# Optimization experiments

Measured on AMD Instinct MI355X. Metric: run time of the kernel, lower is better.

Reference implementation:

```python
import jax, jax.numpy as jnp
import numpy as np
import math

D_MODEL = 1024
NUM_HEADS = 16
D_K = D_MODEL // NUM_HEADS
B, S = 4, 2048


def setup_inputs() -> dict:
    key = jax.random.key(0)
    ks = jax.random.split(key, 12)
    q = jax.random.normal(ks[0], (B, S, D_MODEL), dtype=jnp.float32)
    k = jax.random.normal(ks[1], (B, S, D_MODEL), dtype=jnp.float32)
    v = jax.random.normal(ks[2], (B, S, D_MODEL), dtype=jnp.float32)
    # causal mask: True where attention is disallowed (masked_fill semantics)
    mask = jnp.triu(jnp.ones((S, S), dtype=bool), k=1)
    # xavier_uniform_ for projection weights, torch Linear default for biases
    limit = math.sqrt(6.0 / (D_MODEL + D_MODEL))
    def xavier(kk):
        return jax.random.uniform(kk, (D_MODEL, D_MODEL), jnp.float32, -limit, limit)
    blim = 1.0 / math.sqrt(D_MODEL)
    def bias(kk):
        return jax.random.uniform(kk, (D_MODEL,), jnp.float32, -blim, blim)
    return {
        "q": q, "k": k, "v": v, "mask": mask,
        "wq": xavier(ks[3]), "bq": bias(ks[4]),
        "wk": xavier(ks[5]), "bk": bias(ks[6]),
        "wv": xavier(ks[7]), "bv": bias(ks[8]),
        "wo": xavier(ks[9]), "bo": bias(ks[10]),
    }


def reference(q, k, v, mask, wq, bq, wk, bk, wv, bv, wo, bo):
    b = q.shape[0]
    # torch Linear: y = x @ W.T + b
    def proj(x, w, bb):
        return (jnp.einsum('bsd,ed->bse', x, w) + bb).reshape(b, -1, NUM_HEADS, D_K).transpose(0, 2, 1, 3)
    qh = proj(q, wq, bq)  # [B,H,S,d_k]
    kh = proj(k, wk, bk)
    vh = proj(v, wv, bv)
    scores = jnp.einsum('bhqd,bhkd->bhqk', qh, kh) / math.sqrt(D_K)
    scores = jnp.where(mask, jnp.float32(-1e9), scores)
    probs = jax.nn.softmax(scores, axis=-1)  # dropout p=0 -> identity
    out = jnp.einsum('bhqk,bhkd->bhqd', probs, vh)
    out = out.transpose(0, 2, 1, 3).reshape(b, -1, D_MODEL)
    return jnp.einsum('bsd,ed->bse', out, wo) + bo
```

## Files before the change

kernel.cpp:

```cpp
#include <hip/hip_runtime.h>
#include <hip/hip_bf16.h>
#include <math.h>

#define S_LEN 2048
#define DM    1024
#define NH    16
#define DKH   64
#define NEG_BIG (-1e30f)
#define QSCALE 0.18033688f

typedef __bf16 bf16_t;
typedef bf16_t bf16x8 __attribute__((ext_vector_type(8)));
typedef bf16_t bf16x4 __attribute__((ext_vector_type(4)));
typedef bf16_t bf16x2 __attribute__((ext_vector_type(2)));
typedef float  f32x4  __attribute__((ext_vector_type(4)));

__device__ __forceinline__ void gload16(const void* g, void* l) {
    __builtin_amdgcn_global_load_lds((const __attribute__((address_space(1))) void*)g,
                                     (__attribute__((address_space(3))) void*)l, 16, 0, 0);
}

__device__ __forceinline__ unsigned pack2(float a, float b) {
    bf16x2 v; v[0] = (bf16_t)a; v[1] = (bf16_t)b;
    return __builtin_bit_cast(unsigned, v);
}

__device__ __forceinline__ bf16x8 cvt8v(f32x4 a, f32x4 b) {
    bf16x8 v;
    v[0] = (bf16_t)a[0]; v[1] = (bf16_t)a[1]; v[2] = (bf16_t)a[2]; v[3] = (bf16_t)a[3];
    v[4] = (bf16_t)b[0]; v[5] = (bf16_t)b[1]; v[6] = (bf16_t)b[2]; v[7] = (bf16_t)b[3];
    return v;
}

__global__ __launch_bounds__(256) void cvt4_w(const float* __restrict__ w0, const float* __restrict__ w1,
                                              const float* __restrict__ w2, const float* __restrict__ w3,
                                              bf16_t* __restrict__ o0, bf16_t* __restrict__ o1,
                                              bf16_t* __restrict__ o2, bf16_t* __restrict__ o3) {
    const float* in; bf16_t* out;
    switch (blockIdx.y) {
        case 0: in = w0; out = o0; break;
        case 1: in = w1; out = o1; break;
        case 2: in = w2; out = o2; break;
        default: in = w3; out = o3; break;
    }
    int i = (blockIdx.x * 256 + threadIdx.x) * 4;
    float4 f = *(const float4*)(in + i);
    bf16x4 v;
    v[0] = (bf16_t)f.x; v[1] = (bf16_t)f.y; v[2] = (bf16_t)f.z; v[3] = (bf16_t)f.w;
    *(bf16x4*)(out + i) = v;
}

template<int EPI>
__global__ __launch_bounds__(256) void gemm_proj(const float* __restrict__ Af,
                                                 const bf16_t* __restrict__ B,
                                                 const float* __restrict__ bias,
                                                 bf16_t* __restrict__ Out,
                                                 float oscale) {
    __shared__ float  AsF[128 * 32];
    __shared__ bf16_t Bs[128 * 32];

    const int d    = blockIdx.x;
    const int orig = (d & 7) * 64 + (d >> 3);
    const int mBase = (orig >> 3) * 128;
    const int nBase = (orig & 7) * 128;

    const int tid  = threadIdx.x;
    const int w    = tid >> 6;
    const int lane = tid & 63;
    const int g    = lane >> 4;
    const int r    = lane & 15;
    const int wm   = w >> 1, wn = w & 1;

    const int srow = lane >> 2;
    const int scol = (lane & 3) * 8;
    const int frow = lane >> 3;
    const int fsl  = (lane & 7) ^ (frow & 7);

    f32x4 acc[4][4] = {};

    for (int kt = 0; kt < 1024; kt += 32) {
        #pragma unroll
        for (int c = 0; c < 4; ++c) {
            const int row = w * 32 + c * 8;
            gload16(Af + (size_t)(mBase + row + frow) * 1024 + kt + fsl * 4, &AsF[row * 32]);
        }
        #pragma unroll
        for (int c = 0; c < 2; ++c) {
            const int row = w * 32 + c * 16;
            gload16(B + (size_t)(nBase + row + srow) * 1024 + kt + scol, &Bs[row * 32]);
        }
        __syncthreads();

        bf16x8 af[4], bfr[4];
        #pragma unroll
        for (int i = 0; i < 4; i++) {
            const int R = wm * 64 + i * 16 + r;
            const float* rb = &AsF[R * 32];
            f32x4 f0 = *(const f32x4*)(rb + (((2 * g) ^ (r & 7)) << 2));
            f32x4 f1 = *(const f32x4*)(rb + (((2 * g + 1) ^ (r & 7)) << 2));
            af[i] = cvt8v(f0, f1);
        }
        #pragma unroll
        for (int i = 0; i < 4; i++)
            bfr[i] = *(const bf16x8*)&Bs[(wn * 64 + i * 16 + r) * 32 + g * 8];

        #pragma unroll
        for (int mi = 0; mi < 4; mi++)
            #pragma unroll
            for (int ni = 0; ni < 4; ni++)
                acc[mi][ni] = __builtin_amdgcn_mfma_f32_16x16x32_bf16(
                    af[mi], bfr[ni], acc[mi][ni], 0, 0, 0);
        __syncthreads();
    }

    #pragma unroll
    for (int ni = 0; ni < 4; ni++) {
        const int n = nBase + wn * 64 + ni * 16 + r;
        const float bn = bias[n];
        #pragma unroll
        for (int mi = 0; mi < 4; mi++) {
            #pragma unroll
            for (int qq = 0; qq < 4; qq++) {
                int m = mBase + wm * 64 + mi * 16 + g * 4 + qq;
                float val = (acc[mi][ni][qq] + bn) * oscale;
                int b = m >> 11, s = m & 2047;
                int hh = n >> 6, dd = n & 63;
                bf16_t bvv = (bf16_t)val;
                if constexpr (EPI == 0)
                    Out[(((size_t)(b * NH + hh)) * S_LEN + s) * DKH + dd] = bvv;
                else
                    Out[(((size_t)(b * NH + hh)) * DKH + dd) * S_LEN + s] = bvv;
            }
        }
    }
}

__global__ __launch_bounds__(256) void gemm_o(const bf16_t* __restrict__ A,
                                              const bf16_t* __restrict__ B,
                                              const float* __restrict__ bias,
                                              float* __restrict__ Out) {
    __shared__ bf16_t As[128 * 32];
    __shared__ bf16_t Bs[128 * 32];

    const int d    = blockIdx.x;
    const int orig = (d & 7) * 64 + (d >> 3);
    const int mBase = (orig >> 3) * 128;
    const int nBase = (orig & 7) * 128;

    const int tid  = threadIdx.x;
    const int w    = tid >> 6;
    const int lane = tid & 63;
    const int g    = lane >> 4;
    const int r    = lane & 15;
    const int wm   = w >> 1, wn = w & 1;

    const int srow = lane >> 2;
    const int scol = (lane & 3) * 8;

    f32x4 acc[4][4] = {};

    for (int kt = 0; kt < 1024; kt += 32) {
        #pragma unroll
        for (int c = 0; c < 2; ++c) {
            const int row = w * 32 + c * 16;
            gload16(A + (size_t)(mBase + row + srow) * 1024 + kt + scol, &As[row * 32]);
            gload16(B + (size_t)(nBase + row + srow) * 1024 + kt + scol, &Bs[row * 32]);
        }
        __syncthreads();

        bf16x8 af[4], bfr[4];
        #pragma unroll
        for (int i = 0; i < 4; i++)
            af[i] = *(const bf16x8*)&As[(wm * 64 + i * 16 + r) * 32 + g * 8];
        #pragma unroll
        for (int i = 0; i < 4; i++)
            bfr[i] = *(const bf16x8*)&Bs[(wn * 64 + i * 16 + r) * 32 + g * 8];

        #pragma unroll
        for (int mi = 0; mi < 4; mi++)
            #pragma unroll
            for (int ni = 0; ni < 4; ni++)
                acc[mi][ni] = __builtin_amdgcn_mfma_f32_16x16x32_bf16(
                    af[mi], bfr[ni], acc[mi][ni], 0, 0, 0);
        __syncthreads();
    }

    #pragma unroll
    for (int ni = 0; ni < 4; ni++) {
        const int n = nBase + wn * 64 + ni * 16 + r;
        const float bn = bias[n];
        #pragma unroll
        for (int mi = 0; mi < 4; mi++) {
            #pragma unroll
            for (int qq = 0; qq < 4; qq++) {
                int m = mBase + wm * 64 + mi * 16 + g * 4 + qq;
                Out[(size_t)m * 1024 + n] = acc[mi][ni][qq] + bn;
            }
        }
    }
}

__device__ __forceinline__ void tile_softmax(f32x4 s[4], bool diag, int kbase, int qg,
                                             int g, int srcA, int srcB, bool hi,
                                             bf16x8 pf[2]) {
    unsigned P32[8];
    #pragma unroll
    for (int ni = 0; ni < 4; ++ni) {
        float p[4];
        #pragma unroll
        for (int e = 0; e < 4; ++e) {
            float xx = s[ni][e];
            if (diag) {
                int kk = kbase + ni * 16 + g * 4 + e;
                if (kk > qg) xx = NEG_BIG;
            }
            p[e] = __builtin_amdgcn_exp2f(xx);
        }
        P32[2 * ni]     = pack2(p[0], p[1]);
        P32[2 * ni + 1] = pack2(p[2], p[3]);
    }
    unsigned A0 = __shfl(P32[0], srcA), A1 = __shfl(P32[1], srcA);
    unsigned A2 = __shfl(P32[2], srcA), A3 = __shfl(P32[3], srcA);
    unsigned A4 = __shfl(P32[4], srcA), A5 = __shfl(P32[5], srcA);
    unsigned A6 = __shfl(P32[6], srcA), A7 = __shfl(P32[7], srcA);
    unsigned B0 = __shfl(P32[0], srcB), B1 = __shfl(P32[1], srcB);
    unsigned B2 = __shfl(P32[2], srcB), B3 = __shfl(P32[3], srcB);
    unsigned B4 = __shfl(P32[4], srcB), B5 = __shfl(P32[5], srcB);
    unsigned B6 = __shfl(P32[6], srcB), B7 = __shfl(P32[7], srcB);
    union U { unsigned u[4]; bf16x8 v; } u0, u1;
    u0.u[0] = hi ? A2 : A0;  u0.u[1] = hi ? A3 : A1;
    u0.u[2] = hi ? B2 : B0;  u0.u[3] = hi ? B3 : B1;
    u1.u[0] = hi ? A6 : A4;  u1.u[1] = hi ? A7 : A5;
    u1.u[2] = hi ? B6 : B4;  u1.u[3] = hi ? B7 : B5;
    pf[0] = u0.v;
    pf[1] = u1.v;
}

__global__ __launch_bounds__(256) void attn8_kernel(const bf16_t* __restrict__ Qh,
                                                    const bf16_t* __restrict__ Kh,
                                                    const bf16_t* __restrict__ Vt,
                                                    bf16_t* __restrict__ Out) {
    __shared__ bf16_t KV[2][2][64][64];

    const int j   = blockIdx.x;
    const int c   = j >> 8;
    const int rem = j & 255;
    const int y   = rem >> 6;
    const int bh  = rem & 63;
    const int p   = (c == 0) ? y : (c == 1) ? 15 - y : (c == 2) ? 4 + y : 11 - y;

    const int b   = bh >> 4, h = bh & 15;
    const int tid = threadIdx.x;
    const int w    = tid >> 6;
    const int lane = tid & 63;
    const int g    = lane >> 4;
    const int r    = lane & 15;

    const int qtA = 2 * p, qtB = 2 * p + 1, last = qtB;

    const int srcA = 32 * (g & 1) + r;
    const int srcB = srcA + 16;
    const bool hi  = (g >= 2);

    const bf16_t* Qg = Qh + (size_t)bh * S_LEN * DKH;
    const bf16_t* Kg = Kh + (size_t)bh * S_LEN * DKH;
    const bf16_t* Vg = Vt + (size_t)bh * DKH * S_LEN;

    const int qA = qtA * 64 + w * 16 + r;
    const int qB = qtB * 64 + w * 16 + r;

    bf16x8 qfA[2], qfB[2];
    #pragma unroll
    for (int hh = 0; hh < 2; ++hh) {
        qfA[hh] = *(const bf16x8*)(Qg + (size_t)qA * DKH + hh * 32 + g * 8);
        qfB[hh] = *(const bf16x8*)(Qg + (size_t)qB * DKH + hh * 32 + g * 8);
    }

    bf16x8 ones;
    #pragma unroll
    for (int jj = 0; jj < 8; ++jj) ones[jj] = (bf16_t)1.0f;

    auto stage = [&](int buf, int kt) {
        #pragma unroll
        for (int cc = 0; cc < 2; ++cc) {
            const int row = w * 16 + cc * 8 + (lane >> 3);
            const int sl  = (lane & 7) ^ (row & 7);
            gload16(Kg + ((size_t)(kt * 64 + row)) * DKH + sl * 8,
                    (char*)&KV[buf][0][0][0] + w * 2048 + cc * 1024);
            gload16(Vg + (size_t)row * S_LEN + kt * 64 + sl * 8,
                    (char*)&KV[buf][1][0][0] + w * 2048 + cc * 1024);
        }
    };

    f32x4 oA[4] = {}, oB[4] = {};
    f32x4 lA4 = {}, lB4 = {};

    stage(0, 0);
    asm volatile("s_waitcnt vmcnt(0)" ::: "memory");
    __builtin_amdgcn_s_barrier();

    for (int kt = 0; kt <= last; ++kt) {
        const int buf = kt & 1;
        if (kt < last) stage(buf ^ 1, kt + 1);

        bf16x8 kf[4][2];
        #pragma unroll
        for (int ni = 0; ni < 4; ++ni) {
            const int row = ni * 16 + r;
            const char* base = (const char*)&KV[buf][0][0][0] + (row << 7);
            kf[ni][0] = *(const bf16x8*)(base + (((0 + g) ^ (row & 7)) << 4));
            kf[ni][1] = *(const bf16x8*)(base + (((4 + g) ^ (row & 7)) << 4));
        }

        const bool actA = (kt <= qtA);
        bf16x8 pfA[2], pfB[2];

        if (actA) {
            f32x4 s[4] = {};
            __builtin_amdgcn_s_setprio(1);
            #pragma unroll
            for (int ni = 0; ni < 4; ++ni) {
                s[ni] = __builtin_amdgcn_mfma_f32_16x16x32_bf16(kf[ni][0], qfA[0], s[ni], 0, 0, 0);
                s[ni] = __builtin_amdgcn_mfma_f32_16x16x32_bf16(kf[ni][1], qfA[1], s[ni], 0, 0, 0);
            }
            __builtin_amdgcn_s_setprio(0);
            tile_softmax(s, kt == qtA, kt * 64, qA, g, srcA, srcB, hi, pfA);
        }
        {
            f32x4 s[4] = {};
            __builtin_amdgcn_s_setprio(1);
            #pragma unroll
            for (int ni = 0; ni < 4; ++ni) {
                s[ni] = __builtin_amdgcn_mfma_f32_16x16x32_bf16(kf[ni][0], qfB[0], s[ni], 0, 0, 0);
                s[ni] = __builtin_amdgcn_mfma_f32_16x16x32_bf16(kf[ni][1], qfB[1], s[ni], 0, 0, 0);
            }
            __builtin_amdgcn_s_setprio(0);
            tile_softmax(s, kt == qtB, kt * 64, qB, g, srcA, srcB, hi, pfB);
        }

        __builtin_amdgcn_s_setprio(1);
        #pragma unroll
        for (int ndi = 0; ndi < 4; ++ndi) {
            const int row = ndi * 16 + r;
            const char* base = (const char*)&KV[buf][1][0][0] + (row << 7);
            bf16x8 v0 = *(const bf16x8*)(base + (((0 + g) ^ (row & 7)) << 4));
            bf16x8 v1 = *(const bf16x8*)(base + (((4 + g) ^ (row & 7)) << 4));
            if (actA) {
                oA[ndi] = __builtin_amdgcn_mfma_f32_16x16x32_bf16(v0, pfA[0], oA[ndi], 0, 0, 0);
                oA[ndi] = __builtin_amdgcn_mfma_f32_16x16x32_bf16(v1, pfA[1], oA[ndi], 0, 0, 0);
            }
            oB[ndi] = __builtin_amdgcn_mfma_f32_16x16x32_bf16(v0, pfB[0], oB[ndi], 0, 0, 0);
            oB[ndi] = __builtin_amdgcn_mfma_f32_16x16x32_bf16(v1, pfB[1], oB[ndi], 0, 0, 0);
        }
        if (actA) {
            lA4 = __builtin_amdgcn_mfma_f32_16x16x32_bf16(ones, pfA[0], lA4, 0, 0, 0);
            lA4 = __builtin_amdgcn_mfma_f32_16x16x32_bf16(ones, pfA[1], lA4, 0, 0, 0);
        }
        lB4 = __builtin_amdgcn_mfma_f32_16x16x32_bf16(ones, pfB[0], lB4, 0, 0, 0);
        lB4 = __builtin_amdgcn_mfma_f32_16x16x32_bf16(ones, pfB[1], lB4, 0, 0, 0);
        __builtin_amdgcn_s_setprio(0);

        asm volatile("s_waitcnt vmcnt(0)" ::: "memory");
        __builtin_amdgcn_s_barrier();
    }

    const float invA = 1.0f / lA4[0], invB = 1.0f / lB4[0];
    bf16_t* OutA = Out + ((size_t)(b * S_LEN + qA)) * DM + h * DKH;
    bf16_t* OutB = Out + ((size_t)(b * S_LEN + qB)) * DM + h * DKH;
    #pragma unroll
    for (int ndi = 0; ndi < 4; ++ndi) {
        bf16x4 pa, pb;
        #pragma unroll
        for (int e = 0; e < 4; ++e) {
            pa[e] = (bf16_t)(oA[ndi][e] * invA);
            pb[e] = (bf16_t)(oB[ndi][e] * invB);
        }
        *(bf16x4*)(OutA + ndi * 16 + g * 4) = pa;
        *(bf16x4*)(OutB + ndi * 16 + g * 4) = pb;
    }
}

extern "C" void kernel_launch(void* const* d_in, const int* in_sizes, int n_in,
                              void* d_out, int out_size, void* d_ws, size_t ws_size,
                              hipStream_t stream) {
    const float* q  = (const float*)d_in[0];
    const float* k  = (const float*)d_in[1];
    const float* v  = (const float*)d_in[2];
    const float* wq = (const float*)d_in[4];
    const float* bq = (const float*)d_in[5];
    const float* wk = (const float*)d_in[6];
    const float* bk = (const float*)d_in[7];
    const float* wv = (const float*)d_in[8];
    const float* bv = (const float*)d_in[9];
    const float* wo = (const float*)d_in[10];
    const float* bo = (const float*)d_in[11];
    float* out = (float*)d_out;

    bf16_t* ws   = (bf16_t*)d_ws;
    bf16_t* Wq   = ws;
    bf16_t* Wk   = Wq + (1 << 20);
    bf16_t* Wv   = Wk + (1 << 20);
    bf16_t* Wo   = Wv + (1 << 20);
    bf16_t* Qh   = Wo + (1 << 20);
    bf16_t* Kh   = Qh + (8 << 20);
    bf16_t* Vt   = Kh + (8 << 20);
    bf16_t* attn = Vt + (8 << 20);

    cvt4_w<<<dim3(1024, 4), 256, 0, stream>>>(wq, wk, wv, wo, Wq, Wk, Wv, Wo);

    gemm_proj<0><<<512, 256, 0, stream>>>(q, Wq, bq, Qh, QSCALE);
    gemm_proj<0><<<512, 256, 0, stream>>>(k, Wk, bk, Kh, 1.0f);
    gemm_proj<1><<<512, 256, 0, stream>>>(v, Wv, bv, Vt, 1.0f);

    attn8_kernel<<<1024, 256, 0, stream>>>(Qh, Kh, Vt, attn);

    gemm_o<<<512, 256, 0, stream>>>(attn, Wo, bo, out);
}
```

Before: 193.7 us.

## Double-buffer LDS tiles in projection and output GEMMs to overlap loads

Both the QKV projection GEMM and the output GEMM now use two LDS buffers. The next K-tile is issued through global_load_lds while the MFMAs run on the current one, and each iteration ends with an explicit vmcnt wait and barrier. This is meant to hide global memory latency behind compute, at the cost of doubled LDS use per block, which may reduce occupancy.

```diff
diff --git a/kernel.cpp b/kernel.cpp
--- a/kernel.cpp
+++ b/kernel.cpp
@@ -56,8 +56,8 @@
                                                  const float* __restrict__ bias,
                                                  bf16_t* __restrict__ Out,
                                                  float oscale) {
-    __shared__ float  AsF[128 * 32];
-    __shared__ bf16_t Bs[128 * 32];
+    __shared__ float  AsF[2][128 * 32];
+    __shared__ bf16_t Bs[2][128 * 32];
 
     const int d    = blockIdx.x;
     const int orig = (d & 7) * 64 + (d >> 3);
@@ -76,33 +76,41 @@
     const int frow = lane >> 3;
     const int fsl  = (lane & 7) ^ (frow & 7);
 
-    f32x4 acc[4][4] = {};
-
-    for (int kt = 0; kt < 1024; kt += 32) {
+    auto stage = [&](int buf, int kt) {
         #pragma unroll
         for (int c = 0; c < 4; ++c) {
             const int row = w * 32 + c * 8;
-            gload16(Af + (size_t)(mBase + row + frow) * 1024 + kt + fsl * 4, &AsF[row * 32]);
+            gload16(Af + (size_t)(mBase + row + frow) * 1024 + kt + fsl * 4, &AsF[buf][row * 32]);
         }
         #pragma unroll
         for (int c = 0; c < 2; ++c) {
             const int row = w * 32 + c * 16;
-            gload16(B + (size_t)(nBase + row + srow) * 1024 + kt + scol, &Bs[row * 32]);
-        }
-        __syncthreads();
+            gload16(B + (size_t)(nBase + row + srow) * 1024 + kt + scol, &Bs[buf][row * 32]);
+        }
+    };
+
+    f32x4 acc[4][4] = {};
+
+    stage(0, 0);
+    asm volatile("s_waitcnt vmcnt(0)" ::: "memory");
+    __builtin_amdgcn_s_barrier();
+
+    int cur = 0;
+    for (int kt = 0; kt < 1024; kt += 32) {
+        if (kt + 32 < 1024) stage(cur ^ 1, kt + 32);
 
         bf16x8 af[4], bfr[4];
         #pragma unroll
         for (int i = 0; i < 4; i++) {
             const int R = wm * 64 + i * 16 + r;
-            const float* rb = &AsF[R * 32];
+            const float* rb = &AsF[cur][R * 32];
             f32x4 f0 = *(const f32x4*)(rb + (((2 * g) ^ (r & 7)) << 2));
             f32x4 f1 = *(const f32x4*)(rb + (((2 * g + 1) ^ (r & 7)) << 2));
             af[i] = cvt8v(f0, f1);
         }
         #pragma unroll
         for (int i = 0; i < 4; i++)
-            bfr[i] = *(const bf16x8*)&Bs[(wn * 64 + i * 16 + r) * 32 + g * 8];
+            bfr[i] = *(const bf16x8*)&Bs[cur][(wn * 64 + i * 16 + r) * 32 + g * 8];
 
         #pragma unroll
         for (int mi = 0; mi < 4; mi++)
@@ -110,7 +118,10 @@
             for (int ni = 0; ni < 4; ni++)
                 acc[mi][ni] = __builtin_amdgcn_mfma_f32_16x16x32_bf16(
                     af[mi], bfr[ni], acc[mi][ni], 0, 0, 0);
-        __syncthreads();
+
+        asm volatile("s_waitcnt vmcnt(0)" ::: "memory");
+        __builtin_amdgcn_s_barrier();
+        cur ^= 1;
     }
 
     #pragma unroll
@@ -139,8 +150,8 @@
                                               const bf16_t* __restrict__ B,
                                               const float* __restrict__ bias,
                                               float* __restrict__ Out) {
-    __shared__ bf16_t As[128 * 32];
-    __shared__ bf16_t Bs[128 * 32];
+    __shared__ bf16_t As[2][128 * 32];
+    __shared__ bf16_t Bs[2][128 * 32];
 
     const int d    = blockIdx.x;
     const int orig = (d & 7) * 64 + (d >> 3);
@@ -157,24 +168,32 @@
     const int srow = lane >> 2;
     const int scol = (lane & 3) * 8;
 
-    f32x4 acc[4][4] = {};
-
-    for (int kt = 0; kt < 1024; kt += 32) {
+    auto stage = [&](int buf, int kt) {
         #pragma unroll
         for (int c = 0; c < 2; ++c) {
             const int row = w * 32 + c * 16;
-            gload16(A + (size_t)(mBase + row + srow) * 1024 + kt + scol, &As[row * 32]);
-            gload16(B + (size_t)(nBase + row + srow) * 1024 + kt + scol, &Bs[row * 32]);
-        }
-        __syncthreads();
+            gload16(A + (size_t)(mBase + row + srow) * 1024 + kt + scol, &As[buf][row * 32]);
+            gload16(B + (size_t)(nBase + row + srow) * 1024 + kt + scol, &Bs[buf][row * 32]);
+        }
+    };
+
+    f32x4 acc[4][4] = {};
+
+    stage(0, 0);
+    asm volatile("s_waitcnt vmcnt(0)" ::: "memory");
+    __builtin_amdgcn_s_barrier();
+
+    int cur = 0;
+    for (int kt = 0; kt < 1024; kt += 32) {
+        if (kt + 32 < 1024) stage(cur ^ 1, kt + 32);
 
         bf16x8 af[4], bfr[4];
         #pragma unroll
         for (int i = 0; i < 4; i++)
-            af[i] = *(const bf16x8*)&As[(wm * 64 + i * 16 + r) * 32 + g * 8];
+            af[i] = *(const bf16x8*)&As[cur][(wm * 64 + i * 16 + r) * 32 + g * 8];
         #pragma unroll
         for (int i = 0; i < 4; i++)
-            bfr[i] = *(const bf16x8*)&Bs[(wn * 64 + i * 16 + r) * 32 + g * 8];
+            bfr[i] = *(const bf16x8*)&Bs[cur][(wn * 64 + i * 16 + r) * 32 + g * 8];
 
         #pragma unroll
         for (int mi = 0; mi < 4; mi++)
@@ -182,7 +201,10 @@
             for (int ni = 0; ni < 4; ni++)
                 acc[mi][ni] = __builtin_amdgcn_mfma_f32_16x16x32_bf16(
                     af[mi], bfr[ni], acc[mi][ni], 0, 0, 0);
-        __syncthreads();
+
+        asm volatile("s_waitcnt vmcnt(0)" ::: "memory");
+        __builtin_amdgcn_s_barrier();
+        cur ^= 1;
     }
 
     #pragma unroll
```

After: 192.3 us. Within noise of the previous version (-0.8%).
